# Kernel optimization log

Hardware: AMD Instinct MI355X
Metric: run time of the kernel (lower is better)

## Reference

```python
import jax, jax.numpy as jnp
import numpy as np

B, L, D, E, K, DFF = 2, 2048, 1024, 8, 2, 4096


def setup_inputs() -> dict:
    key = jax.random.key(0)
    kx, kr, kg, ku, kd = jax.random.split(key, 5)
    scale = 0.02
    return {
        "x": jax.random.normal(kx, (B, L, D), dtype=jnp.float32),
        "Wr": jax.random.normal(kr, (E, D), dtype=jnp.float32) * scale,   # router: logits = x @ Wr.T
        "Wg": jax.random.normal(kg, (E, DFF, D), dtype=jnp.float32) * scale,  # gate proj per expert
        "Wu": jax.random.normal(ku, (E, DFF, D), dtype=jnp.float32) * scale,  # up proj per expert
        "Wd": jax.random.normal(kd, (E, D, DFF), dtype=jnp.float32) * scale,  # down proj per expert
    }


def reference(x, Wr, Wg, Wu, Wd):
    Bb, Ll, Dd = x.shape
    T = Bb * Ll
    xt = x.reshape(T, Dd)                                   # [T, D]
    logits = jnp.einsum("td,ed->te", xt, Wr)                # router logits [T, E]
    scores = jax.nn.softmax(logits, axis=-1)
    k_scores, k_ids = jax.lax.top_k(scores, K)              # [T, K]
    eps = jnp.finfo(x.dtype).eps
    k_w = k_scores / (k_scores.sum(axis=-1, keepdims=True) + eps)  # renormalized top-k weights
    # combine[t, e] = sum_k k_w[t, k] * (k_ids[t, k] == e)
    combine = jnp.sum(jax.nn.one_hot(k_ids, E, dtype=x.dtype) * k_w[..., None], axis=1)  # [T, E]
    # GluMLP per expert, computed densely over all tokens (reference form)
    g = jnp.einsum("td,efd->etf", xt, Wg)                   # [E, T, DFF]
    u = jnp.einsum("td,efd->etf", xt, Wu)                   # [E, T, DFF]
    h = jax.nn.relu(g) * u
    out_e = jnp.einsum("etf,edf->etd", h, Wd)               # [E, T, D]
    out = jnp.einsum("te,etd->td", combine, out_e)          # weighted combine [T, D]
    return out.reshape(Bb, Ll, Dd)
```

## Files before the change

### kernel.cpp

```cpp
#include <hip/hip_runtime.h>
#include <hip/hip_bf16.h>

#define Tt 4096
#define Dd 1024
#define Ee 8
#define Kk 2
#define Ff 4096

using f32x4  = __attribute__((ext_vector_type(4))) float;
using bf16x8 = __attribute__((ext_vector_type(8))) short;

__device__ __forceinline__ unsigned short f2bf(float f) {
    union { float fp; unsigned int u; } v; v.fp = f;
    unsigned int u = v.u;
    return (unsigned short)((u + 0x7FFFu + ((u >> 16) & 1u)) >> 16);
}

__device__ __forceinline__ float b2f(unsigned short u) {
    union { float f; unsigned int i; } v; v.i = (unsigned)u << 16; return v.f;
}

__device__ __forceinline__ void gl16(const void* g, void* l) {
    __builtin_amdgcn_global_load_lds(
        (const __attribute__((address_space(1))) void*)g,
        (__attribute__((address_space(3))) void*)l, 16, 0, 0);
}

__global__ void router_kernel(const float* __restrict__ x, const float* __restrict__ Wr,
                              int* __restrict__ ids, float* __restrict__ wts,
                              int* __restrict__ counts, unsigned short* __restrict__ xb) {
    const int t = blockIdx.x;
    const int lane = threadIdx.x;
    const float* xr = x + (size_t)t * Dd + lane * 16;
    float xv[16];
#pragma unroll
    for (int i = 0; i < 4; ++i) *(float4*)(xv + 4 * i) = *(const float4*)(xr + 4 * i);
    uint4 o0, o1;
    o0.x = (unsigned)f2bf(xv[0])  | ((unsigned)f2bf(xv[1])  << 16);
    o0.y = (unsigned)f2bf(xv[2])  | ((unsigned)f2bf(xv[3])  << 16);
    o0.z = (unsigned)f2bf(xv[4])  | ((unsigned)f2bf(xv[5])  << 16);
    o0.w = (unsigned)f2bf(xv[6])  | ((unsigned)f2bf(xv[7])  << 16);
    o1.x = (unsigned)f2bf(xv[8])  | ((unsigned)f2bf(xv[9])  << 16);
    o1.y = (unsigned)f2bf(xv[10]) | ((unsigned)f2bf(xv[11]) << 16);
    o1.z = (unsigned)f2bf(xv[12]) | ((unsigned)f2bf(xv[13]) << 16);
    o1.w = (unsigned)f2bf(xv[14]) | ((unsigned)f2bf(xv[15]) << 16);
    unsigned short* xo = xb + (size_t)t * Dd + lane * 16;
    *(uint4*)(xo) = o0;
    *(uint4*)(xo + 8) = o1;

    double dot[Ee];
#pragma unroll
    for (int e = 0; e < Ee; ++e) {
        const float* wr = Wr + e * Dd + lane * 16;
        double s = 0.0;
#pragma unroll
        for (int i = 0; i < 16; ++i) s += (double)xv[i] * (double)wr[i];
        dot[e] = s;
    }
#pragma unroll
    for (int off = 32; off >= 1; off >>= 1) {
#pragma unroll
        for (int e = 0; e < Ee; ++e) dot[e] += __shfl_xor(dot[e], off, 64);
    }
    if (lane == 0) {
        float lg[Ee];
#pragma unroll
        for (int e = 0; e < Ee; ++e) lg[e] = (float)dot[e];
        float m = lg[0];
        for (int e = 1; e < Ee; ++e) m = fmaxf(m, lg[e]);
        float ex[Ee]; float sum = 0.f;
        for (int e = 0; e < Ee; ++e) { ex[e] = expf(lg[e] - m); sum += ex[e]; }
        float s0 = -1.f, s1 = -1.f; int i0 = 0, i1 = 0;
        for (int e = 0; e < Ee; ++e) {
            float s = ex[e];
            if (s > s0)      { s1 = s0; i1 = i0; s0 = s; i0 = e; }
            else if (s > s1) { s1 = s; i1 = e; }
        }
        float inv = 1.f / sum;
        float sc0 = s0 * inv, sc1 = s1 * inv;
        float den = sc0 + sc1 + 1.1920929e-7f;
        ids[2 * t] = i0; ids[2 * t + 1] = i1;
        wts[2 * t] = sc0 / den; wts[2 * t + 1] = sc1 / den;
        atomicAdd(&counts[i0], 1);
        atomicAdd(&counts[i1], 1);
    }
}

__global__ void cvt_wgu(const float* __restrict__ Wg, const float* __restrict__ Wu,
                        unsigned short* __restrict__ Wgu) {
    size_t tid = (size_t)blockIdx.x * blockDim.x + threadIdx.x;
    size_t row = tid >> 7;
    int dc  = (int)(tid & 127);
    int e   = (int)(row >> 13);
    int j   = (int)(row & 8191);
    int fg = j >> 5, s = (j >> 4) & 1, fi = j & 15;
    int f  = fg * 16 + fi;
    const float* src = (s ? Wu : Wg) + ((size_t)e * Ff + f) * Dd + dc * 8;
    float4 a = *(const float4*)(src);
    float4 b = *(const float4*)(src + 4);
    uint4 o;
    o.x = (unsigned)f2bf(a.x) | ((unsigned)f2bf(a.y) << 16);
    o.y = (unsigned)f2bf(a.z) | ((unsigned)f2bf(a.w) << 16);
    o.z = (unsigned)f2bf(b.x) | ((unsigned)f2bf(b.y) << 16);
    o.w = (unsigned)f2bf(b.z) | ((unsigned)f2bf(b.w) << 16);
    *(uint4*)(Wgu + row * Dd + dc * 8) = o;
}

__global__ void scan_kernel(const int* __restrict__ counts, int* __restrict__ cursor,
                            int* __restrict__ eoff) {
    if (threadIdx.x == 0) {
        int acc = 0;
        for (int e = 0; e < Ee; ++e) { eoff[e] = acc; cursor[e] = acc; acc += counts[e]; }
        eoff[Ee] = acc;
    }
}

__global__ void scatter_kernel(const int* __restrict__ ids,
                               int* __restrict__ cursor, int* __restrict__ rows) {
    int t = blockIdx.x * blockDim.x + threadIdx.x;
    if (t >= Tt) return;
#pragma unroll
    for (int k = 0; k < Kk; ++k) {
        int e = ids[2 * t + k];
        int pos = atomicAdd(&cursor[e], 1);
        rows[pos] = 2 * t + k;
    }
}


#define MFMA_BF16(a, b, c) __builtin_amdgcn_mfma_f32_16x16x32_bf16(a, b, c, 0, 0, 0)

template<bool G2>
__device__ __forceinline__ void gemm_body(unsigned short* Ls,
                                          const unsigned short* __restrict__ Abase,
                                          const unsigned short* __restrict__ Bbase,
                                          const int* __restrict__ eoff,
                                          const int* __restrict__ rows,
                                          unsigned short* __restrict__ H,
                                          unsigned short* __restrict__ partial) {
    constexpr int KLEN  = G2 ? Ff : Dd;
    constexpr int NT    = (G2 ? 2048 : 1024) / 64;
    constexpr int MT    = G2 ? 128 : 256;
    constexpr int BN    = G2 ? 128 : 256;
    constexpr int MFR   = MT / 32;
    constexpr int NF    = BN / 64;
    constexpr int AISS  = MT / 64;
    constexpr int BISS  = BN / 64;
    constexpr int AH0   = AISS / 2;
    constexpr int BH0   = BISS / 2;
    constexpr int ABUFU = MT * 64;
    constexpr int BBUFU = BN * 64;
    constexpr int BBASE = 2 * ABUFU;
    const int e   = blockIdx.z;
    const int off = eoff[e];
    const int ne  = eoff[e + 1] - off;
    const int by  = blockIdx.y;
    const int my  = G2 ? (by >> 1) : by;
    const int sK  = G2 ? (by & 1) : 0;
    const int koff = sK * 2048;
    const int m0  = my * MT;
    if (m0 >= ne) return;
    const int n0  = blockIdx.x * BN;

    const int tid  = threadIdx.x;
    const int lane = tid & 63;
    const int w    = tid >> 6;
    const int wr   = w >> 2;
    const int wc   = w & 3;
    const int lr   = lane & 15;
    const int lc   = lane >> 4;

    const int sr = lane >> 3;
    const int cA = (lane & 7) ^ sr;
    int asrc[AISS];
#pragma unroll
    for (int j = 0; j < AISS; ++j) {
        int rr = m0 + j * 64 + w * 8 + sr;
        if (rr > ne - 1) rr = ne - 1;
        asrc[j] = (G2 ? (off + rr) : (rows[off + rr] >> 1)) * KLEN + cA * 8;
    }
    const unsigned short* Bp = Bbase + (size_t)e * (G2 ? (size_t)Dd * Ff : (size_t)8192 * Dd);
    int bsrc[BISS];
#pragma unroll
    for (int j = 0; j < BISS; ++j) {
        int rN = n0 + j * 64 + w * 8 + sr;
        bsrc[j] = rN * KLEN + cA * 8;
    }

    auto STAGE_A = [&](int T, int half) {
        const int bo_ = (T & 1) * ABUFU; const int kt_ = koff + T * 64;
        if (half == 0) {
#pragma unroll
            for (int j = 0; j < AH0; ++j)
                gl16(Abase + asrc[j] + kt_, Ls + bo_ + j * 4096 + w * 512);
        } else {
#pragma unroll
            for (int j = AH0; j < AISS; ++j)
                gl16(Abase + asrc[j] + kt_, Ls + bo_ + j * 4096 + w * 512);
        }
    };
    auto STAGE_B = [&](int T, int half) {
        const int bo_ = BBASE + (T & 1) * BBUFU; const int kt_ = koff + T * 64;
        if (half == 0) {
#pragma unroll
            for (int j = 0; j < BH0; ++j)
                gl16(Bp + bsrc[j] + kt_, Ls + bo_ + j * 4096 + w * 512);
        } else {
#pragma unroll
            for (int j = BH0; j < BISS; ++j)
                gl16(Bp + bsrc[j] + kt_, Ls + bo_ + j * 4096 + w * 512);
        }
    };

#define WAIT_STEADY() do { if constexpr (G2) { asm volatile("s_waitcnt vmcnt(2)" ::: "memory"); } \
                           else              { asm volatile("s_waitcnt vmcnt(4)" ::: "memory"); } } while (0)

    const int ccx0 = ((0 * 4 + lc) ^ (lr & 7)) * 8;
    const int ccx1 = ((1 * 4 + lc) ^ (lr & 7)) * 8;
    const int aB = (wr * (MT / 2)) * 64 + lr * 64;
    const int bB = BBASE + (wc * (BN / 4)) * 64 + lr * 64;

    f32x4 acc[MFR][NF];
#pragma unroll
    for (int m = 0; m < MFR; ++m)
#pragma unroll
        for (int n = 0; n < NF; ++n) acc[m][n] = (f32x4){0.f, 0.f, 0.f, 0.f};

    STAGE_A(0, 0); STAGE_A(0, 1); STAGE_B(0, 0); STAGE_B(0, 1);
    STAGE_A(1, 0); STAGE_A(1, 1);
    WAIT_STEADY();
    __builtin_amdgcn_sched_barrier(0);
    __builtin_amdgcn_s_barrier();

    bf16x8 a0[MFR], a1[MFR], b0[NF], b1[NF];

    for (int t = 0; t < NT; ++t) {
        const int abo = (t & 1) * ABUFU;
        const int bbo = (t & 1) * BBUFU;
#pragma unroll
        for (int m = 0; m < MFR; ++m) a0[m] = *(const bf16x8*)(Ls + abo + aB + m * 1024 + ccx0);
#pragma unroll
        for (int n = 0; n < NF; ++n) b0[n] = *(const bf16x8*)(Ls + bbo + bB + n * 1024 + ccx0);
        if (t + 1 < NT) STAGE_B(t + 1, 0);
        __builtin_amdgcn_s_barrier();
        asm volatile("s_waitcnt lgkmcnt(0)" ::: "memory");
        __builtin_amdgcn_sched_barrier(0);
        __builtin_amdgcn_s_setprio(1);
#pragma unroll
        for (int m = 0; m < MFR; ++m)
#pragma unroll
            for (int n = 0; n < NF / 2; ++n)
                acc[m][n] = MFMA_BF16(a0[m], b0[n], acc[m][n]);
        __builtin_amdgcn_s_setprio(0);
        __builtin_amdgcn_s_barrier();
#pragma unroll
        for (int m = 0; m < MFR; ++m) a1[m] = *(const bf16x8*)(Ls + abo + aB + m * 1024 + ccx1);
        if (t + 1 < NT) STAGE_B(t + 1, 1);
        __builtin_amdgcn_s_barrier();
        __builtin_amdgcn_s_setprio(1);
#pragma unroll
        for (int m = 0; m < MFR; ++m)
#pragma unroll
            for (int n = NF / 2; n < NF; ++n)
                acc[m][n] = MFMA_BF16(a0[m], b0[n], acc[m][n]);
        __builtin_amdgcn_s_setprio(0);
        asm volatile("s_waitcnt lgkmcnt(0)" ::: "memory");
        __builtin_amdgcn_sched_barrier(0);
        __builtin_amdgcn_s_barrier();
#pragma unroll
        for (int n = 0; n < NF; ++n) b1[n] = *(const bf16x8*)(Ls + bbo + bB + n * 1024 + ccx1);
        if (t + 2 < NT) STAGE_A(t + 2, 0);
        __builtin_amdgcn_s_barrier();
        asm volatile("s_waitcnt lgkmcnt(0)" ::: "memory");
        __builtin_amdgcn_sched_barrier(0);
        __builtin_amdgcn_s_setprio(1);
#pragma unroll
        for (int m = 0; m < MFR; ++m)
#pragma unroll
            for (int n = 0; n < NF / 2; ++n)
                acc[m][n] = MFMA_BF16(a1[m], b1[n], acc[m][n]);
        __builtin_amdgcn_s_setprio(0);
        __builtin_amdgcn_s_barrier();
        if (t + 2 < NT) STAGE_A(t + 2, 1);
        __builtin_amdgcn_s_setprio(1);
#pragma unroll
        for (int m = 0; m < MFR; ++m)
#pragma unroll
            for (int n = NF / 2; n < NF; ++n)
                acc[m][n] = MFMA_BF16(a1[m], b1[n], acc[m][n]);
        __builtin_amdgcn_s_setprio(0);
        if (t + 2 < NT) { WAIT_STEADY(); }
        else            { asm volatile("s_waitcnt vmcnt(0)" ::: "memory"); }
        __builtin_amdgcn_sched_barrier(0);
        __builtin_amdgcn_s_barrier();
    }

    if constexpr (!G2) {
        const int fg16 = ((n0 + wc * 64) >> 5) * 16 + lr;
#pragma unroll
        for (int m = 0; m < MFR; ++m) {
            const int itok = m0 + wr * (MT / 2) + m * 16 + lc * 4;
#pragma unroll
            for (int r = 0; r < 4; ++r) {
                const int i = itok + r;
                if (i < ne) {
                    unsigned short* hp = H + (size_t)(off + i) * Ff;
#pragma unroll
                    for (int np = 0; np < 2; ++np) {
                        const float g = acc[m][2 * np][r];
                        const float u = acc[m][2 * np + 1][r];
                        hp[fg16 + np * 16] = f2bf(fmaxf(g, 0.f) * u);
                    }
                }
            }
        }
    } else {
        const int dbase = n0 + wc * (BN / 4);
#pragma unroll
        for (int m = 0; m < MFR; ++m) {
            const int ib = m0 + wr * (MT / 2) + m * 16 + lc * 4;
#pragma unroll
            for (int r = 0; r < 4; ++r) {
                const int i = ib + r;
                if (i < ne) {
                    const int tr = rows[off + i];
                    unsigned short* op = partial + ((size_t)sK * 8192 + tr) * Dd + dbase + lr;
#pragma unroll
                    for (int n = 0; n < NF; ++n) op[n * 16] = f2bf(acc[m][n][r]);
                }
            }
        }
    }
#undef WAIT_STEADY
}

__global__ __launch_bounds__(512, 1)
void g1_moe(const unsigned short* __restrict__ xb, const unsigned short* __restrict__ Wgu,
            const int* __restrict__ eoff, const int* __restrict__ rows,
            unsigned short* __restrict__ H,
            const float* __restrict__ Wd, unsigned short* __restrict__ Wdb) {
    __shared__ __align__(16) unsigned short Ls[65536];
    gemm_body<false>(Ls, xb, Wgu, eoff, rows, H, nullptr);
    const int fb = blockIdx.x + gridDim.x * (blockIdx.y + gridDim.y * blockIdx.z);
    const size_t base = (size_t)fb * 8192;
#pragma unroll
    for (int it = 0; it < 2; ++it) {
        const size_t i = base + (size_t)it * 4096 + threadIdx.x * 8;
        float4 a = *(const float4*)(Wd + i);
        float4 b = *(const float4*)(Wd + i + 4);
        uint4 o;
        o.x = (unsigned)f2bf(a.x) | ((unsigned)f2bf(a.y) << 16);
        o.y = (unsigned)f2bf(a.z) | ((unsigned)f2bf(a.w) << 16);
        o.z = (unsigned)f2bf(b.x) | ((unsigned)f2bf(b.y) << 16);
        o.w = (unsigned)f2bf(b.z) | ((unsigned)f2bf(b.w) << 16);
        *(uint4*)(Wdb + i) = o;
    }
}

__global__ __launch_bounds__(512, 1)
void g2_moe(const unsigned short* __restrict__ H, const unsigned short* __restrict__ Wdb,
            const int* __restrict__ eoff, const int* __restrict__ rows,
            unsigned short* __restrict__ partial) {
    __shared__ __align__(16) unsigned short Ls[32768];
    gemm_body<true>(Ls, H, Wdb, eoff, rows, nullptr, partial);
}

__global__ void reduce_kernel(const unsigned short* __restrict__ P, const float* __restrict__ wts,
                              float* __restrict__ out) {
    const size_t idx = (size_t)blockIdx.x * blockDim.x + threadIdx.x;
    const size_t t  = idx >> 7;
    const int   dq  = (int)(idx & 127);
    const float w0 = wts[2 * t], w1 = wts[2 * t + 1];
    const unsigned short* p00 = P + ((size_t)(2 * t))            * Dd + dq * 8;
    const unsigned short* p01 = P + ((size_t)(2 * t + 1))        * Dd + dq * 8;
    const unsigned short* p10 = P + ((size_t)8192 + 2 * t)       * Dd + dq * 8;
    const unsigned short* p11 = P + ((size_t)8192 + 2 * t + 1)   * Dd + dq * 8;
    bf16x8 a = *(const bf16x8*)p00;
    bf16x8 b = *(const bf16x8*)p01;
    bf16x8 c = *(const bf16x8*)p10;
    bf16x8 d = *(const bf16x8*)p11;
    float o[8];
#pragma unroll
    for (int j = 0; j < 8; ++j)
        o[j] = w0 * (b2f((unsigned short)a[j]) + b2f((unsigned short)c[j]))
             + w1 * (b2f((unsigned short)b[j]) + b2f((unsigned short)d[j]));
    float* op = out + t * Dd + dq * 8;
    *(float4*)(op)     = (float4){o[0], o[1], o[2], o[3]};
    *(float4*)(op + 4) = (float4){o[4], o[5], o[6], o[7]};
}

extern "C" void kernel_launch(void* const* d_in, const int* in_sizes, int n_in,
                              void* d_out, int out_size, void* d_ws, size_t ws_size,
                              hipStream_t stream) {
    const float* x  = (const float*)d_in[0];
    const float* Wr = (const float*)d_in[1];
    const float* Wg = (const float*)d_in[2];
    const float* Wu = (const float*)d_in[3];
    const float* Wd = (const float*)d_in[4];
    float* out = (float*)d_out;
    char* ws = (char*)d_ws;

    const size_t WELEM    = (size_t)Ee * Ff * Dd;
    const size_t OFF_IDS  = 256;
    const size_t OFF_WTS  = OFF_IDS  + (size_t)Tt * 2 * 4;
    const size_t OFF_ROWS = OFF_WTS  + (size_t)Tt * 2 * 4;
    const size_t OFF_ROWW = OFF_ROWS + (size_t)Tt * Kk * 4;
    const size_t OFF_XB   = OFF_ROWW + (size_t)Tt * Kk * 4;
    const size_t OFF_H    = OFF_XB   + (size_t)Tt * Dd * 2;
    const size_t OFF_WGU  = OFF_H    + (size_t)Tt * Kk * Ff * 2;
    const size_t OFF_WD   = OFF_WGU  + WELEM * 2 * 2;
    const size_t NEED     = OFF_WD   + WELEM * 2;
    if (ws_size < NEED) return;

    int* counts = (int*)ws;
    int* cursor = (int*)(ws + 32);
    int* eoff   = (int*)(ws + 64);
    int* ids    = (int*)(ws + OFF_IDS);
    float* wts  = (float*)(ws + OFF_WTS);
    int* rows   = (int*)(ws + OFF_ROWS);
    unsigned short* xb  = (unsigned short*)(ws + OFF_XB);
    unsigned short* H   = (unsigned short*)(ws + OFF_H);
    unsigned short* Wgu = (unsigned short*)(ws + OFF_WGU);
    unsigned short* Wdb = (unsigned short*)(ws + OFF_WD);
    unsigned short* partial = (unsigned short*)(ws + OFF_WGU);

    hipMemsetAsync(ws, 0, 256, stream);

    router_kernel  <<<Tt, 64, 0, stream>>>(x, Wr, ids, wts, counts, xb);
    scan_kernel    <<<1, 64, 0, stream>>>(counts, cursor, eoff);
    scatter_kernel <<<Tt / 256, 256, 0, stream>>>(ids, cursor, rows);

    cvt_wgu        <<<32768, 256, 0, stream>>>(Wg, Wu, Wgu);

    g1_moe <<<dim3(2 * Ff / 256, Tt / 256, Ee), 512, 0, stream>>>(
        xb, Wgu, eoff, rows, H, Wd, Wdb);
    g2_moe <<<dim3(Dd / 128, 20, Ee), 512, 0, stream>>>(
        H, Wdb, eoff, rows, partial);

    reduce_kernel  <<<(Tt * Dd / 8) / 256, 256, 0, stream>>>(partial, wts, out);
}
```

Measured before the change: 496.2 us.

## Fuse gate/up weight bf16 conversion into grouped GEMM B-tile loading

Drops the separate cvt_wgu pass that converted the fp32 Wg/Wu weights into an interleaved bf16 buffer. The first grouped GEMM now loads fp32 weights into registers, converts them to bf16 and writes them to LDS inside its software pipeline. This removes a full read-and-write pass over the gate/up weights and one kernel launch. In exchange, each M-tile block now re-reads fp32 weights (twice the bytes) through the register path instead of async global-to-LDS loads, and it adds register pressure and extra waits.

```diff
diff --git a/kernel.cpp b/kernel.cpp
--- a/kernel.cpp
+++ b/kernel.cpp
@@ -86,26 +86,6 @@
     }
 }
 
-__global__ void cvt_wgu(const float* __restrict__ Wg, const float* __restrict__ Wu,
-                        unsigned short* __restrict__ Wgu) {
-    size_t tid = (size_t)blockIdx.x * blockDim.x + threadIdx.x;
-    size_t row = tid >> 7;
-    int dc  = (int)(tid & 127);
-    int e   = (int)(row >> 13);
-    int j   = (int)(row & 8191);
-    int fg = j >> 5, s = (j >> 4) & 1, fi = j & 15;
-    int f  = fg * 16 + fi;
-    const float* src = (s ? Wu : Wg) + ((size_t)e * Ff + f) * Dd + dc * 8;
-    float4 a = *(const float4*)(src);
-    float4 b = *(const float4*)(src + 4);
-    uint4 o;
-    o.x = (unsigned)f2bf(a.x) | ((unsigned)f2bf(a.y) << 16);
-    o.y = (unsigned)f2bf(a.z) | ((unsigned)f2bf(a.w) << 16);
-    o.z = (unsigned)f2bf(b.x) | ((unsigned)f2bf(b.y) << 16);
-    o.w = (unsigned)f2bf(b.z) | ((unsigned)f2bf(b.w) << 16);
-    *(uint4*)(Wgu + row * Dd + dc * 8) = o;
-}
-
 __global__ void scan_kernel(const int* __restrict__ counts, int* __restrict__ cursor,
                             int* __restrict__ eoff) {
     if (threadIdx.x == 0) {
@@ -134,6 +114,8 @@
 __device__ __forceinline__ void gemm_body(unsigned short* Ls,
                                           const unsigned short* __restrict__ Abase,
                                           const unsigned short* __restrict__ Bbase,
+                                          const float* __restrict__ WgF,
+                                          const float* __restrict__ WuF,
                                           const int* __restrict__ eoff,
                                           const int* __restrict__ rows,
                                           unsigned short* __restrict__ H,
@@ -145,9 +127,7 @@
     constexpr int MFR   = MT / 32;
     constexpr int NF    = BN / 64;
     constexpr int AISS  = MT / 64;
-    constexpr int BISS  = BN / 64;
     constexpr int AH0   = AISS / 2;
-    constexpr int BH0   = BISS / 2;
     constexpr int ABUFU = MT * 64;
     constexpr int BBUFU = BN * 64;
     constexpr int BBASE = 2 * ABUFU;
@@ -179,12 +159,25 @@
         if (rr > ne - 1) rr = ne - 1;
         asrc[j] = (G2 ? (off + rr) : (rows[off + rr] >> 1)) * KLEN + cA * 8;
     }
-    const unsigned short* Bp = Bbase + (size_t)e * (G2 ? (size_t)Dd * Ff : (size_t)8192 * Dd);
-    int bsrc[BISS];
-#pragma unroll
-    for (int j = 0; j < BISS; ++j) {
-        int rN = n0 + j * 64 + w * 8 + sr;
-        bsrc[j] = rN * KLEN + cA * 8;
+
+    const unsigned short* Bp = nullptr;
+    int bsrc[2];
+    const float* bptr[4];
+    if constexpr (G2) {
+        Bp = Bbase + (size_t)e * (size_t)Dd * Ff;
+#pragma unroll
+        for (int j = 0; j < 2; ++j) {
+            int rN = n0 + j * 64 + w * 8 + sr;
+            bsrc[j] = rN * KLEN + cA * 8;
+        }
+    } else {
+#pragma unroll
+        for (int j = 0; j < 4; ++j) {
+            int vr = n0 + j * 64 + w * 8 + sr;
+            int fg = vr >> 5, sgu = (vr >> 4) & 1, fi = vr & 15;
+            int f  = fg * 16 + fi;
+            bptr[j] = (sgu ? WuF : WgF) + ((size_t)e * Ff + f) * Dd + cA * 8;
+        }
     }
 
     auto STAGE_A = [&](int T, int half) {
@@ -199,16 +192,30 @@
                 gl16(Abase + asrc[j] + kt_, Ls + bo_ + j * 4096 + w * 512);
         }
     };
-    auto STAGE_B = [&](int T, int half) {
+    auto STAGE_B2 = [&](int T, int half) {
         const int bo_ = BBASE + (T & 1) * BBUFU; const int kt_ = koff + T * 64;
-        if (half == 0) {
-#pragma unroll
-            for (int j = 0; j < BH0; ++j)
-                gl16(Bp + bsrc[j] + kt_, Ls + bo_ + j * 4096 + w * 512);
-        } else {
-#pragma unroll
-            for (int j = BH0; j < BISS; ++j)
-                gl16(Bp + bsrc[j] + kt_, Ls + bo_ + j * 4096 + w * 512);
+        gl16(Bp + bsrc[half] + kt_, Ls + bo_ + half * 4096 + w * 512);
+    };
+    float4 bld[4][2];
+    auto LOAD_B = [&](int T, int Hh) {
+#pragma unroll
+        for (int jj = 0; jj < 2; ++jj) {
+            const int j = 2 * Hh + jj;
+            const float* p = bptr[j] + T * 64;
+            bld[j][0] = *(const float4*)(p);
+            bld[j][1] = *(const float4*)(p + 4);
+        }
+    };
+    auto WRITE_B = [&](int T) {
+        const int bo_ = BBASE + (T & 1) * BBUFU;
+#pragma unroll
+        for (int j = 0; j < 4; ++j) {
+            uint4 o;
+            o.x = (unsigned)f2bf(bld[j][0].x) | ((unsigned)f2bf(bld[j][0].y) << 16);
+            o.y = (unsigned)f2bf(bld[j][0].z) | ((unsigned)f2bf(bld[j][0].w) << 16);
+            o.z = (unsigned)f2bf(bld[j][1].x) | ((unsigned)f2bf(bld[j][1].y) << 16);
+            o.w = (unsigned)f2bf(bld[j][1].z) | ((unsigned)f2bf(bld[j][1].w) << 16);
+            *(uint4*)(Ls + bo_ + j * 4096 + w * 512 + lane * 8) = o;
         }
     };
 
@@ -226,9 +233,20 @@
 #pragma unroll
         for (int n = 0; n < NF; ++n) acc[m][n] = (f32x4){0.f, 0.f, 0.f, 0.f};
 
-    STAGE_A(0, 0); STAGE_A(0, 1); STAGE_B(0, 0); STAGE_B(0, 1);
-    STAGE_A(1, 0); STAGE_A(1, 1);
-    WAIT_STEADY();
+    if constexpr (G2) {
+        STAGE_A(0, 0); STAGE_A(0, 1); STAGE_B2(0, 0); STAGE_B2(0, 1);
+        STAGE_A(1, 0); STAGE_A(1, 1);
+        WAIT_STEADY();
+    } else {
+        LOAD_B(0, 0); LOAD_B(0, 1);
+        STAGE_A(0, 0); STAGE_A(0, 1);
+        STAGE_A(1, 0); STAGE_A(1, 1);
+        asm volatile("s_waitcnt vmcnt(4)" ::: "memory");
+        __builtin_amdgcn_sched_barrier(0);
+        WRITE_B(0);
+        LOAD_B(1, 0); LOAD_B(1, 1);
+        asm volatile("s_waitcnt lgkmcnt(0)" ::: "memory");
+    }
     __builtin_amdgcn_sched_barrier(0);
     __builtin_amdgcn_s_barrier();
 
@@ -241,7 +259,8 @@
         for (int m = 0; m < MFR; ++m) a0[m] = *(const bf16x8*)(Ls + abo + aB + m * 1024 + ccx0);
 #pragma unroll
         for (int n = 0; n < NF; ++n) b0[n] = *(const bf16x8*)(Ls + bbo + bB + n * 1024 + ccx0);
-        if (t + 1 < NT) STAGE_B(t + 1, 0);
+        if constexpr (G2) { if (t + 1 < NT) STAGE_B2(t + 1, 0); }
+        else              { if (t >= 1 && t + 1 < NT) LOAD_B(t + 1, 0); }
         __builtin_amdgcn_s_barrier();
         asm volatile("s_waitcnt lgkmcnt(0)" ::: "memory");
         __builtin_amdgcn_sched_barrier(0);
@@ -255,7 +274,8 @@
         __builtin_amdgcn_s_barrier();
 #pragma unroll
         for (int m = 0; m < MFR; ++m) a1[m] = *(const bf16x8*)(Ls + abo + aB + m * 1024 + ccx1);
-        if (t + 1 < NT) STAGE_B(t + 1, 1);
+        if constexpr (G2) { if (t + 1 < NT) STAGE_B2(t + 1, 1); }
+        else              { if (t >= 1 && t + 1 < NT) LOAD_B(t + 1, 1); }
         __builtin_amdgcn_s_barrier();
         __builtin_amdgcn_s_setprio(1);
 #pragma unroll
@@ -291,6 +311,11 @@
         __builtin_amdgcn_s_setprio(0);
         if (t + 2 < NT) { WAIT_STEADY(); }
         else            { asm volatile("s_waitcnt vmcnt(0)" ::: "memory"); }
+        __builtin_amdgcn_sched_barrier(0);
+        if constexpr (!G2) {
+            if (t + 1 < NT) WRITE_B(t + 1);
+            asm volatile("s_waitcnt lgkmcnt(0)" ::: "memory");
+        }
         __builtin_amdgcn_sched_barrier(0);
         __builtin_amdgcn_s_barrier();
     }
@@ -335,12 +360,13 @@
 }
 
 __global__ __launch_bounds__(512, 1)
-void g1_moe(const unsigned short* __restrict__ xb, const unsigned short* __restrict__ Wgu,
+void g1_moe(const unsigned short* __restrict__ xb,
+            const float* __restrict__ Wg, const float* __restrict__ Wu,
             const int* __restrict__ eoff, const int* __restrict__ rows,
             unsigned short* __restrict__ H,
             const float* __restrict__ Wd, unsigned short* __restrict__ Wdb) {
     __shared__ __align__(16) unsigned short Ls[65536];
-    gemm_body<false>(Ls, xb, Wgu, eoff, rows, H, nullptr);
+    gemm_body<false>(Ls, xb, nullptr, Wg, Wu, eoff, rows, H, nullptr);
     const int fb = blockIdx.x + gridDim.x * (blockIdx.y + gridDim.y * blockIdx.z);
     const size_t base = (size_t)fb * 8192;
 #pragma unroll
@@ -362,7 +388,7 @@
             const int* __restrict__ eoff, const int* __restrict__ rows,
             unsigned short* __restrict__ partial) {
     __shared__ __align__(16) unsigned short Ls[32768];
-    gemm_body<true>(Ls, H, Wdb, eoff, rows, nullptr, partial);
+    gemm_body<true>(Ls, H, Wdb, nullptr, nullptr, eoff, rows, nullptr, partial);
 }
 
 __global__ void reduce_kernel(const unsigned short* __restrict__ P, const float* __restrict__ wts,
@@ -371,10 +397,10 @@
     const size_t t  = idx >> 7;
     const int   dq  = (int)(idx & 127);
     const float w0 = wts[2 * t], w1 = wts[2 * t + 1];
-    const unsigned short* p00 = P + ((size_t)(2 * t))            * Dd + dq * 8;
-    const unsigned short* p01 = P + ((size_t)(2 * t + 1))        * Dd + dq * 8;
-    const unsigned short* p10 = P + ((size_t)8192 + 2 * t)       * Dd + dq * 8;
-    const unsigned short* p11 = P + ((size_t)8192 + 2 * t + 1)   * Dd + dq * 8;
+    const unsigned short* p00 = P + ((size_t)(2 * t))          * Dd + dq * 8;
+    const unsigned short* p01 = P + ((size_t)(2 * t + 1))      * Dd + dq * 8;
+    const unsigned short* p10 = P + ((size_t)8192 + 2 * t)     * Dd + dq * 8;
+    const unsigned short* p11 = P + ((size_t)8192 + 2 * t + 1) * Dd + dq * 8;
     bf16x8 a = *(const bf16x8*)p00;
     bf16x8 b = *(const bf16x8*)p01;
     bf16x8 c = *(const bf16x8*)p10;
@@ -420,7 +446,6 @@
     int* rows   = (int*)(ws + OFF_ROWS);
     unsigned short* xb  = (unsigned short*)(ws + OFF_XB);
     unsigned short* H   = (unsigned short*)(ws + OFF_H);
-    unsigned short* Wgu = (unsigned short*)(ws + OFF_WGU);
     unsigned short* Wdb = (unsigned short*)(ws + OFF_WD);
     unsigned short* partial = (unsigned short*)(ws + OFF_WGU);
 
@@ -430,10 +455,8 @@
     scan_kernel    <<<1, 64, 0, stream>>>(counts, cursor, eoff);
     scatter_kernel <<<Tt / 256, 256, 0, stream>>>(ids, cursor, rows);
 
-    cvt_wgu        <<<32768, 256, 0, stream>>>(Wg, Wu, Wgu);
-
     g1_moe <<<dim3(2 * Ff / 256, Tt / 256, Ee), 512, 0, stream>>>(
-        xb, Wgu, eoff, rows, H, Wd, Wdb);
+        xb, Wg, Wu, eoff, rows, H, Wd, Wdb);
     g2_moe <<<dim3(Dd / 128, 20, Ee), 512, 0, stream>>>(
         H, Wdb, eoff, rows, partial);
 
```

Result: slower. 631.5 us (+27.3%).
